# Kernel tuning notes

Hardware: AMD Instinct MI355X
Metric: run time of the kernel (lower is better)

## Reference

```python
import jax, jax.numpy as jnp
import numpy as np

N = 50000
E = 800000
H = 128
L = 3
EPS_BN = 1e-5
EPS_NORM = 1e-12
NEG_SLOPE = 0.1


def setup_inputs() -> dict:
    key = jax.random.key(0)
    ks = jax.random.split(key, 10)
    s = 1.0 / np.sqrt(H)
    x = jax.random.normal(ks[0], (N, H), dtype=jnp.float32)
    edge_index = jax.random.randint(ks[1], (2, E), 0, N, dtype=jnp.int64)
    # per-layer SAGEConv params: lin_l (neighbors, with bias), lin_r (root, no bias)
    Wl = jax.random.uniform(ks[2], (L, H, H), jnp.float32, -s, s)
    bl = jax.random.uniform(ks[3], (L, H), jnp.float32, -s, s)
    Wr = jax.random.uniform(ks[4], (L, H, H), jnp.float32, -s, s)
    # BatchNorm affine params per layer
    gamma = jnp.ones((L, H), jnp.float32)
    beta = jnp.zeros((L, H), jnp.float32)
    # shared skip linear
    Ws = jax.random.uniform(ks[5], (H, H), jnp.float32, -s, s)
    bs = jax.random.uniform(ks[6], (H,), jnp.float32, -s, s)
    return {"x": x, "edge_index": edge_index, "Wl": Wl, "bl": bl, "Wr": Wr,
            "gamma": gamma, "beta": beta, "Ws": Ws, "bs": bs}


def _layer(x, src, dst, Wl, bl, Wr, g, b, Ws, bs):
    # skip residual
    res = x @ Ws.T + bs
    # SAGEConv mean aggregation: messages src -> dst
    agg = jax.ops.segment_sum(x[src], dst, num_segments=N)  # [N,H]
    deg = jax.ops.segment_sum(jnp.ones((E,), x.dtype), dst, num_segments=N)
    agg = agg / jnp.maximum(deg, 1.0)[:, None]
    out = agg @ Wl.T + bl + x @ Wr.T
    # normalize=True -> L2 normalize over features
    nrm = jnp.sqrt(jnp.sum(out * out, axis=-1, keepdims=True))
    out = out / jnp.maximum(nrm, EPS_NORM)
    # BatchNorm over nodes (batch statistics)
    mu = out.mean(axis=0)
    var = out.var(axis=0)
    out = (out - mu) * jax.lax.rsqrt(var + EPS_BN) * g + b
    # LeakyReLU(0.1); dropout is identity in eval
    out = jnp.where(out >= 0, out, NEG_SLOPE * out)
    return out + res


def reference(x, edge_index, Wl, bl, Wr, gamma, beta, Ws, bs):
    src, dst = edge_index[0], edge_index[1]
    for l in range(L):
        x = _layer(x, src, dst, Wl[l], bl[l], Wr[l], gamma[l], beta[l], Ws, bs)
    return x
```

## Files before the change

kernel.cpp:

```cpp
#include <hip/hip_runtime.h>
#include <hip/hip_bf16.h>
#include <stdint.h>

#define NN 50000
#define NE 800000
#define HD 128
#define NL 3
#define EPS_BN 1e-5f
#define EPS_NORM 1e-12f
#define NEG_SLOPE 0.1f

#define SCAN_CHUNK 256
#define SCAN_BLOCKS ((NN + SCAN_CHUNK - 1) / SCAN_CHUNK)
#define NTILES ((NN + 127) / 128)

typedef __attribute__((ext_vector_type(8))) short bf16x8;
typedef __attribute__((ext_vector_type(4))) float f32x4;

static __device__ __forceinline__ unsigned pack_bf16(float a, float b) {
  unsigned ua = __builtin_bit_cast(unsigned, a);
  unsigned ub = __builtin_bit_cast(unsigned, b);
  ua = (ua + 0x7fffu + ((ua >> 16) & 1u)) >> 16;
  ub = (ub + 0x7fffu + ((ub >> 16) & 1u)) >> 16;
  return ua | (ub << 16);
}
static __device__ __forceinline__ ushort bf16of(float f) {
  unsigned u = __builtin_bit_cast(unsigned, f);
  u = (u + 0x7fffu + ((u >> 16) & 1u)) >> 16;
  return (ushort)u;
}
static __device__ __forceinline__ float bflo(unsigned u) { return __builtin_bit_cast(float, u << 16); }
static __device__ __forceinline__ float bfhi(unsigned u) { return __builtin_bit_cast(float, u & 0xffff0000u); }

__global__ __launch_bounds__(256) void hist_kernel(const int* __restrict__ dst, int* __restrict__ degi) {
  int i = blockIdx.x * 256 + threadIdx.x;
  if (i < NE) atomicAdd(&degi[dst[i]], 1);
}

__global__ __launch_bounds__(256) void blocksum_kernel(const int* __restrict__ degi,
                                                       int* __restrict__ blocksum) {
  __shared__ int sh[256];
  int t = threadIdx.x;
  int i = blockIdx.x * 256 + t;
  sh[t] = (i < NN) ? degi[i] : 0;
  __syncthreads();
  for (int off = 128; off >= 1; off >>= 1) {
    if (t < off) sh[t] += sh[t + off];
    __syncthreads();
  }
  if (t == 0) blocksum[blockIdx.x] = sh[0];
}

__global__ __launch_bounds__(256) void blockscan_kernel(int* __restrict__ blocksum,
                                                        int* __restrict__ blockoff,
                                                        int* __restrict__ rowptr) {
  __shared__ int sh[256];
  int t = threadIdx.x;
  int v = (t < SCAN_BLOCKS) ? blocksum[t] : 0;
  sh[t] = v;
  __syncthreads();
  for (int off = 1; off < 256; off <<= 1) {
    int u = (t >= off) ? sh[t - off] : 0;
    __syncthreads();
    sh[t] += u;
    __syncthreads();
  }
  if (t < SCAN_BLOCKS) blockoff[t] = sh[t] - v;
  if (t == 255) rowptr[NN] = sh[255];
}

__global__ __launch_bounds__(256) void chunkscan_kernel(const int* __restrict__ degi,
                                                        const int* __restrict__ blockoff,
                                                        int* __restrict__ rowptr,
                                                        int* __restrict__ cursor,
                                                        float* __restrict__ invdeg) {
  __shared__ int sh[256];
  int t = threadIdx.x;
  int i = blockIdx.x * 256 + t;
  int d = (i < NN) ? degi[i] : 0;
  sh[t] = d;
  __syncthreads();
  for (int off = 1; off < 256; off <<= 1) {
    int u = (t >= off) ? sh[t - off] : 0;
    __syncthreads();
    sh[t] += u;
    __syncthreads();
  }
  if (i < NN) {
    int pre = blockoff[blockIdx.x] + sh[t] - d;
    rowptr[i] = pre;
    cursor[i] = pre;
    invdeg[i] = 1.0f / fmaxf((float)d, 1.0f);
  }
}

__global__ __launch_bounds__(256) void fill_kernel(const int* __restrict__ src,
                                                   const int* __restrict__ dst,
                                                   int* __restrict__ cursor,
                                                   int* __restrict__ esrc) {
  int e = blockIdx.x * 256 + threadIdx.x;
  if (e < NE) {
    int pos = atomicAdd(&cursor[dst[e]], 1);
    esrc[pos] = src[e];
  }
}

__global__ __launch_bounds__(256) void tobf16_kernel(const float* __restrict__ x, ushort* __restrict__ xb) {
  int i = blockIdx.x * 256 + threadIdx.x;
  if (i < NN * 64) {
    float2 f = *(const float2*)(x + (size_t)i * 2);
    *(unsigned*)(xb + (size_t)i * 2) = pack_bf16(f.x, f.y);
  }
}

__global__ __launch_bounds__(256) void packW_kernel(const float* __restrict__ Wl,
                                                    const float* __restrict__ Wr,
                                                    const float* __restrict__ Wsm,
                                                    unsigned* __restrict__ wpackL,
                                                    unsigned* __restrict__ wpackS) {
  int i = blockIdx.x * 256 + threadIdx.x;
  if (i < NL * 16384) {
    int l = i >> 14, rem = i & 16383;
    int c = rem >> 7, kp = rem & 127;
    int k2 = kp * 2;
    float f0, f1;
    if (k2 < HD) { const float* W = Wl + (size_t)l * HD * HD + c * HD + k2; f0 = W[0]; f1 = W[1]; }
    else         { const float* W = Wr + (size_t)l * HD * HD + c * HD + (k2 - HD); f0 = W[0]; f1 = W[1]; }
    unsigned ba = (unsigned)(c * 512 + kp * 4) ^ (unsigned)((c & 7) << 4);
    *(unsigned*)((char*)(wpackL + (size_t)l * 16384) + ba) = pack_bf16(f0, f1);
  } else if (i < NL * 16384 + 8192) {
    int j = i - NL * 16384;
    int c = j >> 6, kp = j & 63;
    int k2 = kp * 2;
    unsigned ba = (unsigned)(c * 256 + kp * 4) ^ (unsigned)((c & 7) << 4);
    *(unsigned*)((char*)wpackS + ba) = pack_bf16(Wsm[c * HD + k2], Wsm[c * HD + k2 + 1]);
  }
}

__global__ __launch_bounds__(512) void agg_csr_kernel(const ushort* __restrict__ xb,
                                                      const int* __restrict__ rowptr,
                                                      const int* __restrict__ esrc,
                                                      const float* __restrict__ invdeg,
                                                      ushort* __restrict__ aggb,
                                                      float* __restrict__ colsum,
                                                      float* __restrict__ colsumsq) {
  if (blockIdx.x == 0 && threadIdx.x < 2 * HD) {
    if (threadIdx.x < HD) colsum[threadIdx.x] = 0.f;
    else colsumsq[threadIdx.x - HD] = 0.f;
  }
  int wid = (blockIdx.x * 512 + threadIdx.x) >> 6;
  int lane = threadIdx.x & 63;
  int half = lane >> 5, sub = lane & 31;
  int node = wid * 2 + half;
  if (node >= NN) return;
  int start = rowptr[node], end = rowptr[node + 1];
  float a0 = 0.f, a1 = 0.f, a2 = 0.f, a3 = 0.f;
  int e = start;
  for (; e + 4 <= end; e += 4) {
    int s0 = esrc[e], s1 = esrc[e + 1], s2 = esrc[e + 2], s3 = esrc[e + 3];
    uint2 u0 = *(const uint2*)((const char*)xb + (size_t)s0 * 256 + sub * 8);
    uint2 u1 = *(const uint2*)((const char*)xb + (size_t)s1 * 256 + sub * 8);
    uint2 u2 = *(const uint2*)((const char*)xb + (size_t)s2 * 256 + sub * 8);
    uint2 u3 = *(const uint2*)((const char*)xb + (size_t)s3 * 256 + sub * 8);
    a0 += (bflo(u0.x) + bflo(u1.x)) + (bflo(u2.x) + bflo(u3.x));
    a1 += (bfhi(u0.x) + bfhi(u1.x)) + (bfhi(u2.x) + bfhi(u3.x));
    a2 += (bflo(u0.y) + bflo(u1.y)) + (bflo(u2.y) + bflo(u3.y));
    a3 += (bfhi(u0.y) + bfhi(u1.y)) + (bfhi(u2.y) + bfhi(u3.y));
  }
  for (; e < end; ++e) {
    uint2 u = *(const uint2*)((const char*)xb + (size_t)esrc[e] * 256 + sub * 8);
    a0 += bflo(u.x);
    a1 += bfhi(u.x);
    a2 += bflo(u.y);
    a3 += bfhi(u.y);
  }
  float id = invdeg[node];
  uint2 o;
  o.x = pack_bf16(a0 * id, a1 * id);
  o.y = pack_bf16(a2 * id, a3 * id);
  *(uint2*)((char*)aggb + (size_t)node * 256 + sub * 8) = o;
}

__global__ __launch_bounds__(512, 4) void mfma_pre_kernel(
    const ushort* __restrict__ aggb, const ushort* __restrict__ xb,
    const unsigned* __restrict__ wpackL, const float* __restrict__ bl,
    uint4* __restrict__ prebn,
    float* __restrict__ colsum, float* __restrict__ colsumsq) {
  __shared__ unsigned Bsw[16384];
  __shared__ float lsum[HD], lsq[HD];
  const int tid = threadIdx.x;
  {
    const uint4* s = (const uint4*)wpackL;
    uint4* d = (uint4*)Bsw;
#pragma unroll
    for (int i = 0; i < 8; ++i) d[tid + i * 512] = s[tid + i * 512];
  }
  if (tid < HD) { lsum[tid] = 0.f; lsq[tid] = 0.f; }

  const int wave = tid >> 6, lane = tid & 63;
  const int lhi = lane >> 4, llo = lane & 15;
  int arow = blockIdx.x * 128 + wave * 16 + llo;
  if (arow >= NN) arow = NN - 1;
  const size_t rb = (size_t)arow * 256;

  uint4 areg[8];
#pragma unroll
  for (int ks = 0; ks < 4; ++ks) {
    areg[ks]     = *(const uint4*)((const char*)aggb + rb + ks * 64 + lhi * 16);
    areg[ks + 4] = *(const uint4*)((const char*)xb   + rb + ks * 64 + lhi * 16);
  }

  f32x4 acc[8];
#pragma unroll
  for (int ct = 0; ct < 8; ++ct) {
    float b = bl[ct * 16 + llo];
    acc[ct] = (f32x4){b, b, b, b};
  }
  __syncthreads();

#pragma unroll
  for (int ks = 0; ks < 8; ++ks) {
    bf16x8 a = __builtin_bit_cast(bf16x8, areg[ks]);
#pragma unroll
    for (int ct = 0; ct < 8; ++ct) {
      int bcol = ct * 16 + llo;
      unsigned bb = (unsigned)(bcol * 512 + ks * 64 + lhi * 16) ^ (unsigned)((bcol & 7) << 4);
      bf16x8 b = *(const bf16x8*)((const char*)Bsw + bb);
      acc[ct] = __builtin_amdgcn_mfma_f32_16x16x32_bf16(a, b, acc[ct], 0, 0, 0);
    }
  }

  float cs[8] = {0, 0, 0, 0, 0, 0, 0, 0}, cq[8] = {0, 0, 0, 0, 0, 0, 0, 0};
#pragma unroll
  for (int r = 0; r < 4; ++r) {
    int orow = blockIdx.x * 128 + wave * 16 + lhi * 4 + r;
    float p[8];
    float ss = 0.f;
#pragma unroll
    for (int ct = 0; ct < 8; ++ct) { p[ct] = acc[ct][r]; ss += p[ct] * p[ct]; }
#pragma unroll
    for (int m = 8; m >= 1; m >>= 1) ss += __shfl_xor(ss, m, 64);
    float inv = 1.0f / fmaxf(sqrtf(ss), EPS_NORM);
#pragma unroll
    for (int ct = 0; ct < 8; ++ct) p[ct] *= inv;
    uint4 o;
    o.x = pack_bf16(p[0], p[1]);
    o.y = pack_bf16(p[2], p[3]);
    o.z = pack_bf16(p[4], p[5]);
    o.w = pack_bf16(p[6], p[7]);
    prebn[((size_t)blockIdx.x * 32 + wave * 4 + r) * 64 + lane] = o;
    if (orow < NN) {
#pragma unroll
      for (int ct = 0; ct < 8; ++ct) { cs[ct] += p[ct]; cq[ct] += p[ct] * p[ct]; }
    }
  }
#pragma unroll
  for (int ct = 0; ct < 8; ++ct) {
    atomicAdd(&lsum[ct * 16 + llo], cs[ct]);
    atomicAdd(&lsq[ct * 16 + llo], cq[ct]);
  }
  __syncthreads();
  if (tid < HD) {
    atomicAdd(&colsum[tid], lsum[tid]);
    atomicAdd(&colsumsq[tid], lsq[tid]);
  }
}

__global__ __launch_bounds__(512, 4) void res_mfma_kernel(
    ushort* __restrict__ xb, const uint4* __restrict__ prebn,
    const unsigned* __restrict__ wpackS, const float* __restrict__ bs,
    const float* __restrict__ colsum, const float* __restrict__ colsumsq,
    const float* __restrict__ gamma, const float* __restrict__ beta,
    float* __restrict__ outf, int last) {
  __shared__ unsigned Bsw[8192];
  __shared__ float lscale[HD], lshift[HD];
  const int tid = threadIdx.x;
  {
    const uint4* s = (const uint4*)wpackS;
    uint4* d = (uint4*)Bsw;
#pragma unroll
    for (int i = 0; i < 4; ++i) d[tid + i * 512] = s[tid + i * 512];
  }
  if (tid < HD) {
    float mu = colsum[tid] * (1.0f / NN);
    float ex2 = colsumsq[tid] * (1.0f / NN);
    float var = ex2 - mu * mu;
    float sc = gamma[tid] * rsqrtf(var + EPS_BN);
    lscale[tid] = sc;
    lshift[tid] = beta[tid] - mu * sc;
  }

  const int wave = tid >> 6, lane = tid & 63;
  const int lhi = lane >> 4, llo = lane & 15;
  int arow = blockIdx.x * 128 + wave * 16 + llo;
  if (arow >= NN) arow = NN - 1;
  const size_t rb = (size_t)arow * 256;

  uint4 areg[4];
#pragma unroll
  for (int ks = 0; ks < 4; ++ks)
    areg[ks] = *(const uint4*)((const char*)xb + rb + ks * 64 + lhi * 16);
  uint4 pv4[4];
#pragma unroll
  for (int r = 0; r < 4; ++r)
    pv4[r] = prebn[((size_t)blockIdx.x * 32 + wave * 4 + r) * 64 + lane];

  f32x4 acc[8];
#pragma unroll
  for (int ct = 0; ct < 8; ++ct) {
    float b = bs[ct * 16 + llo];
    acc[ct] = (f32x4){b, b, b, b};
  }
  __syncthreads();

  float sc8[8], sh8[8];
#pragma unroll
  for (int ct = 0; ct < 8; ++ct) {
    int C = ct * 16 + llo;
    sc8[ct] = lscale[C];
    sh8[ct] = lshift[C];
  }

#pragma unroll
  for (int ks = 0; ks < 4; ++ks) {
    bf16x8 a = __builtin_bit_cast(bf16x8, areg[ks]);
#pragma unroll
    for (int ct = 0; ct < 8; ++ct) {
      int bcol = ct * 16 + llo;
      unsigned bb = (unsigned)(bcol * 256 + ks * 64 + lhi * 16) ^ (unsigned)((bcol & 7) << 4);
      bf16x8 b = *(const bf16x8*)((const char*)Bsw + bb);
      acc[ct] = __builtin_amdgcn_mfma_f32_16x16x32_bf16(a, b, acc[ct], 0, 0, 0);
    }
  }

#pragma unroll
  for (int r = 0; r < 4; ++r) {
    int orow = blockIdx.x * 128 + wave * 16 + lhi * 4 + r;
    if (orow < NN) {
      const unsigned* pw = (const unsigned*)&pv4[r];
#pragma unroll
      for (int ct = 0; ct < 8; ++ct) {
        unsigned w = pw[ct >> 1];
        float pv = (ct & 1) ? bfhi(w) : bflo(w);
        float v = pv * sc8[ct] + sh8[ct];
        v = v >= 0.f ? v : NEG_SLOPE * v;
        float o = v + acc[ct][r];
        if (last) outf[(size_t)orow * HD + ct * 16 + llo] = o;
        else      xb[(size_t)orow * HD + ct * 16 + llo] = bf16of(o);
      }
    }
  }
}

extern "C" void kernel_launch(void* const* d_in, const int* in_sizes, int n_in,
                              void* d_out, int out_size, void* d_ws, size_t ws_size,
                              hipStream_t stream) {
  const float* x0    = (const float*)d_in[0];
  const int*   ei    = (const int*)d_in[1];
  const float* Wl    = (const float*)d_in[2];
  const float* bl    = (const float*)d_in[3];
  const float* Wr    = (const float*)d_in[4];
  const float* gamma = (const float*)d_in[5];
  const float* beta  = (const float*)d_in[6];
  const float* Wsm   = (const float*)d_in[7];
  const float* bs    = (const float*)d_in[8];
  float* out = (float*)d_out;

  char* w = (char*)d_ws;
  ushort* aggb = (ushort*)w;        w += (size_t)NN * HD * 2;
  ushort* xb   = (ushort*)w;        w += (size_t)NN * HD * 2;
  uint4* prebn = (uint4*)w;         w += (size_t)NTILES * 32 * 64 * 16;
  unsigned* wpackL = (unsigned*)w;  w += (size_t)NL * 16384 * 4;
  unsigned* wpackS = (unsigned*)w;  w += 8192 * 4;
  float* invdeg = (float*)w;        w += (size_t)NN * 4;
  float* colsum = (float*)w;        w += HD * 4;
  float* colsumsq = (float*)w;      w += HD * 4;
  int* degi = (int*)w;              w += (size_t)NN * 4;
  int* rowptr = (int*)w;            w += (size_t)(NN + 1) * 4;
  int* cursor = (int*)w;            w += (size_t)NN * 4;
  int* blocksum = (int*)w;          w += SCAN_BLOCKS * 4;
  int* blockoff = (int*)w;          w += SCAN_BLOCKS * 4;
  int* esrc = (int*)w;              w += (size_t)NE * 4;

  const int* srcp = ei;
  const int* dstp = ei + NE;

  hipMemsetAsync(degi, 0, NN * sizeof(int), stream);
  hist_kernel<<<(NE + 255) / 256, 256, 0, stream>>>(dstp, degi);
  blocksum_kernel<<<SCAN_BLOCKS, 256, 0, stream>>>(degi, blocksum);
  blockscan_kernel<<<1, 256, 0, stream>>>(blocksum, blockoff, rowptr);
  chunkscan_kernel<<<SCAN_BLOCKS, 256, 0, stream>>>(degi, blockoff, rowptr, cursor, invdeg);
  fill_kernel<<<(NE + 255) / 256, 256, 0, stream>>>(srcp, dstp, cursor, esrc);
  tobf16_kernel<<<(NN * 64 + 255) / 256, 256, 0, stream>>>(x0, xb);
  packW_kernel<<<(NL * 16384 + 8192 + 255) / 256, 256, 0, stream>>>(Wl, Wr, Wsm, wpackL, wpackS);

  const int aggBlocks = ((NN + 1) / 2 * 64 + 511) / 512;
  for (int l = 0; l < NL; ++l) {
    agg_csr_kernel<<<aggBlocks, 512, 0, stream>>>(xb, rowptr, esrc, invdeg, aggb,
                                                  colsum, colsumsq);
    mfma_pre_kernel<<<NTILES, 512, 0, stream>>>(aggb, xb, wpackL + (size_t)l * 16384,
                                                bl + (size_t)l * HD, prebn, colsum, colsumsq);
    res_mfma_kernel<<<NTILES, 512, 0, stream>>>(xb, prebn, wpackS, bs,
                                                colsum, colsumsq,
                                                gamma + (size_t)l * HD, beta + (size_t)l * HD,
                                                out, l == NL - 1 ? 1 : 0);
  }
}
```

Measured before the change: 341.0 us.

## Replace atomic CSR fill with two-pass bucketed sort through shared memory

The CSR build no longer does one global atomic per edge on per-node cursors with scattered writes. It first groups edges into 512-node buckets: each block builds a local histogram, reserves space with one atomic per bucket and writes coalesced (src,dst) pairs. A second kernel then places each bucket's edges by node in shared memory and writes esrc contiguously. The aim is less global atomic contention and more coalesced writes, at the cost of an extra intermediate buffer, an extra kernel and a fixed MAXBE shared-memory cap that could overflow if a bucket has too many edges.

```diff
diff --git a/kernel.cpp b/kernel.cpp
--- a/kernel.cpp
+++ b/kernel.cpp
@@ -14,6 +14,10 @@
 #define SCAN_BLOCKS ((NN + SCAN_CHUNK - 1) / SCAN_CHUNK)
 #define NTILES ((NN + 127) / 128)
 
+#define BSH 9
+#define NB ((NN + (1 << BSH) - 1) >> BSH)
+#define MAXBE 9728
+
 typedef __attribute__((ext_vector_type(8))) short bf16x8;
 typedef __attribute__((ext_vector_type(4))) float f32x4;
 
@@ -72,7 +76,7 @@
 __global__ __launch_bounds__(256) void chunkscan_kernel(const int* __restrict__ degi,
                                                         const int* __restrict__ blockoff,
                                                         int* __restrict__ rowptr,
-                                                        int* __restrict__ cursor,
+                                                        int* __restrict__ bcursor,
                                                         float* __restrict__ invdeg) {
   __shared__ int sh[256];
   int t = threadIdx.x;
@@ -89,20 +93,69 @@
   if (i < NN) {
     int pre = blockoff[blockIdx.x] + sh[t] - d;
     rowptr[i] = pre;
-    cursor[i] = pre;
+    if ((i & ((1 << BSH) - 1)) == 0) bcursor[i >> BSH] = pre;
     invdeg[i] = 1.0f / fmaxf((float)d, 1.0f);
   }
 }
 
-__global__ __launch_bounds__(256) void fill_kernel(const int* __restrict__ src,
-                                                   const int* __restrict__ dst,
-                                                   int* __restrict__ cursor,
-                                                   int* __restrict__ esrc) {
-  int e = blockIdx.x * 256 + threadIdx.x;
-  if (e < NE) {
-    int pos = atomicAdd(&cursor[dst[e]], 1);
-    esrc[pos] = src[e];
-  }
+__global__ __launch_bounds__(1024) void bucketB_kernel(const int* __restrict__ src,
+                                                       const int* __restrict__ dst,
+                                                       int* __restrict__ bcursor,
+                                                       uint2* __restrict__ bpack) {
+  __shared__ int hist[NB], lstart[NB], gbase[NB];
+  __shared__ uint2 sdat[1024];
+  const int tid = threadIdx.x;
+  const int e = blockIdx.x * 1024 + tid;
+  if (tid < NB) hist[tid] = 0;
+  __syncthreads();
+  int s = 0, d = 0, b = 0, myIdx = 0;
+  bool valid = (e < NE);
+  if (valid) {
+    s = src[e];
+    d = dst[e];
+    b = d >> BSH;
+    myIdx = atomicAdd(&hist[b], 1);
+  }
+  __syncthreads();
+  if (tid == 0) {
+    int run = 0;
+    for (int i = 0; i < NB; ++i) { lstart[i] = run; run += hist[i]; }
+  }
+  __syncthreads();
+  if (tid < NB && hist[tid] > 0) gbase[tid] = atomicAdd(&bcursor[tid], hist[tid]);
+  __syncthreads();
+  if (valid) sdat[lstart[b] + myIdx] = make_uint2((unsigned)s, (unsigned)d);
+  __syncthreads();
+  int tot = lstart[NB - 1] + hist[NB - 1];
+  if (tid < tot) {
+    uint2 p = sdat[tid];
+    int bb = (int)(p.y >> BSH);
+    bpack[gbase[bb] + (tid - lstart[bb])] = p;
+  }
+}
+
+__global__ __launch_bounds__(1024) void bucketC_kernel(const int* __restrict__ rowptr,
+                                                       const uint2* __restrict__ bpack,
+                                                       int* __restrict__ esrc) {
+  __shared__ int lcur[1 << BSH];
+  __shared__ int lsrc[MAXBE];
+  const int c = blockIdx.x, tid = threadIdx.x;
+  const int nbase = c << BSH;
+  const int nend = min(nbase + (1 << BSH), NN);
+  const int ebase = rowptr[nbase];
+  const int cnt = rowptr[nend] - ebase;
+  if (tid < (1 << BSH)) {
+    int n = nbase + tid;
+    lcur[tid] = (n < nend) ? rowptr[n] - ebase : 0;
+  }
+  __syncthreads();
+  for (int i = tid; i < cnt; i += 1024) {
+    uint2 p = bpack[ebase + i];
+    int pos = atomicAdd(&lcur[(int)p.y - nbase], 1);
+    if (pos < MAXBE) lsrc[pos] = (int)p.x;
+  }
+  __syncthreads();
+  for (int i = tid; i < cnt; i += 1024) esrc[ebase + i] = lsrc[i];
 }
 
 __global__ __launch_bounds__(256) void tobf16_kernel(const float* __restrict__ x, ushort* __restrict__ xb) {
@@ -377,9 +430,10 @@
   float* colsumsq = (float*)w;      w += HD * 4;
   int* degi = (int*)w;              w += (size_t)NN * 4;
   int* rowptr = (int*)w;            w += (size_t)(NN + 1) * 4;
-  int* cursor = (int*)w;            w += (size_t)NN * 4;
+  int* bcursor = (int*)w;           w += (size_t)(NB + 8) * 4;
   int* blocksum = (int*)w;          w += SCAN_BLOCKS * 4;
   int* blockoff = (int*)w;          w += SCAN_BLOCKS * 4;
+  uint2* bpack = (uint2*)w;         w += (size_t)NE * 8;
   int* esrc = (int*)w;              w += (size_t)NE * 4;
 
   const int* srcp = ei;
@@ -389,8 +443,9 @@
   hist_kernel<<<(NE + 255) / 256, 256, 0, stream>>>(dstp, degi);
   blocksum_kernel<<<SCAN_BLOCKS, 256, 0, stream>>>(degi, blocksum);
   blockscan_kernel<<<1, 256, 0, stream>>>(blocksum, blockoff, rowptr);
-  chunkscan_kernel<<<SCAN_BLOCKS, 256, 0, stream>>>(degi, blockoff, rowptr, cursor, invdeg);
-  fill_kernel<<<(NE + 255) / 256, 256, 0, stream>>>(srcp, dstp, cursor, esrc);
+  chunkscan_kernel<<<SCAN_BLOCKS, 256, 0, stream>>>(degi, blockoff, rowptr, bcursor, invdeg);
+  bucketB_kernel<<<(NE + 1023) / 1024, 1024, 0, stream>>>(srcp, dstp, bcursor, bpack);
+  bucketC_kernel<<<NB, 1024, 0, stream>>>(rowptr, bpack, esrc);
   tobf16_kernel<<<(NN * 64 + 255) / 256, 256, 0, stream>>>(x0, xb);
   packW_kernel<<<(NL * 16384 + 8192 + 255) / 256, 256, 0, stream>>>(Wl, Wr, Wsm, wpackL, wpackS);
 
```

New measurement: 317.6 us. -6.9%, faster.
